# Optimization experiments

Measured on AMD Instinct MI355X. Metric: run time of the kernel, lower is better.

The kernel has to match this reference:

```python
import jax, jax.numpy as jnp
import numpy as np

C = 1.0          # curvature
MIN_NORM = 1e-15
EPS = 1e-7       # atanh clamp for fp32

def _sqnorm(x):
    return jnp.sum(x * x, axis=-1, keepdims=True)

def _norm(x):
    return jnp.sqrt(jnp.maximum(_sqnorm(x), MIN_NORM))

def _atanh(u):
    return jnp.arctanh(jnp.clip(u, -1.0 + EPS, 1.0 - EPS))

def mobius_add(x, y, c):
    x2 = _sqnorm(x); y2 = _sqnorm(y)
    xy = jnp.sum(x * y, axis=-1, keepdims=True)
    num = (1.0 + 2.0 * c * xy + c * y2) * x + (1.0 - c * x2) * y
    den = 1.0 + 2.0 * c * xy + c * c * x2 * y2
    return num / jnp.maximum(den, MIN_NORM)

def logmap0(p, c):
    sc = jnp.sqrt(c)
    pn = _norm(p)
    return p / pn / sc * _atanh(sc * pn)

def logmap(p1, p2, c):
    # tangent vector at p1 pointing to p2 (Poincare ball)
    sub = mobius_add(-p1, p2, c)
    sn = _norm(sub)
    lam = 2.0 / jnp.maximum(1.0 - c * _sqnorm(p1), MIN_NORM)
    sc = jnp.sqrt(c)
    return 2.0 / sc / lam * _atanh(sc * sn) * sub / sn

def expmap(p, u, c):
    un = _norm(u)
    lam = 2.0 / jnp.maximum(1.0 - c * _sqnorm(p), MIN_NORM)
    sc = jnp.sqrt(c)
    second = jnp.tanh(sc * lam * un / 2.0) * u / (sc * un)
    return mobius_add(p, second, c)


def setup_inputs() -> dict:
    key = jax.random.key(0)
    k1, k2, k3 = jax.random.split(key, 3)
    B, N, D = 1, 1024, 128
    # points inside the unit Poincare ball (||x|| ~ 0.23)
    x = jax.random.normal(k1, (B, N, D), jnp.float32) * 0.02
    # sparse-ish dense adjacency mask (0/1 floats)
    adj = (jax.random.uniform(k2, (B, N, N)) < 0.05).astype(jnp.float32)
    # DenseAtt: nn.Linear(2*D, 1) weight (flattened) + bias
    att_w = jax.random.normal(k3, (2 * D,), jnp.float32) * 0.1
    att_b = jnp.zeros((), jnp.float32)
    return {"x": x, "adj": adj, "att_w": att_w, "att_b": att_b}


def reference(x, adj, att_w, att_b):
    B, N, D = x.shape
    x_t = logmap0(x, C)                                   # [B,N,D]
    # DenseAtt: sigmoid(Linear(cat(x_i, x_j))) decomposed as left_i + right_j + b
    left = x_t @ att_w[:D]                                # [B,N]
    right = x_t @ att_w[D:]                               # [B,N]
    att = jax.nn.sigmoid(left[:, :, None] + right[:, None, :] + att_b) * adj  # [B,N,N]
    # pairwise logmap: tangent at x_i of every x_j  -> [B,N,N,D]
    x_local = logmap(x[:, :, None, :], x[:, None, :, :], C)
    support_t = jnp.einsum('bij,bijd->bid', att, x_local)  # [B,N,D]
    return expmap(x, support_t, C)
```

## Files before the change

### kernel.cpp

```cpp
#include <hip/hip_runtime.h>
#include <math.h>


typedef short short4v __attribute__((ext_vector_type(4)));
typedef short short8v __attribute__((ext_vector_type(8)));
typedef float float4v __attribute__((ext_vector_type(4)));

static __device__ __forceinline__ short f2bf(float f) {
    unsigned u = __float_as_uint(f);
    u += 0x7fff + ((u >> 16) & 1);
    return (short)(u >> 16);
}
static __device__ __forceinline__ float rcpf(float x) { return __builtin_amdgcn_rcpf(x); }
static __device__ __forceinline__ short8v ld8(const unsigned short* p) {
    short4v lo = *(const short4v*)p;
    short4v hi = *(const short4v*)(p + 4);
    return (short8v){lo[0],lo[1],lo[2],lo[3],hi[0],hi[1],hi[2],hi[3]};
}
static __device__ __forceinline__ float dot4(float4v a, float4v b) {
    return a[0]*b[0] + a[1]*b[1] + a[2]*b[2] + a[3]*b[3];
}
static __device__ __forceinline__ float atanh_over(float pn) {
    float uu = fminf(pn, 1.f - 1e-7f);
    return 0.5f * __logf((1.f + uu) * rcpf(1.f - uu)) * rcpf(pn);
}

__global__ __launch_bounds__(256) void hyp_prep(
    const float* __restrict__ x, const float* __restrict__ w,
    const float* __restrict__ battp,
    unsigned short* __restrict__ Xb, unsigned short* __restrict__ Xbt,
    float* __restrict__ st_x2, float* __restrict__ st_L, float* __restrict__ st_R)
{
    __shared__ unsigned short sT[128 * 20];
    __shared__ float sPx[16 * 36], sPl[16 * 36], sPr[16 * 36];
    const int t  = threadIdx.x;
    const int r0 = blockIdx.x * 16;
    const float4v* x4 = (const float4v*)x;
    const float4v* w4 = (const float4v*)w;

#pragma unroll
    for (int it = 0; it < 2; ++it) {
        int bid = t + it * 256;
        int jr = bid >> 5, dc = bid & 31;
        float4v v  = x4[(r0 + jr) * 32 + dc];
        float4v w1 = w4[dc], w2 = w4[32 + dc];
        short4v h = { f2bf(v[0]), f2bf(v[1]), f2bf(v[2]), f2bf(v[3]) };
        *(short4v*)&Xb[(r0 + jr) * 128 + dc * 4] = h;
#pragma unroll
        for (int d = 0; d < 4; ++d)
            sT[(dc * 4 + d) * 20 + jr] = (unsigned short)h[d];
        sPx[jr * 36 + dc] = dot4(v, v);
        sPl[jr * 36 + dc] = dot4(v, w1);
        sPr[jr * 36 + dc] = dot4(v, w2);
    }
    __syncthreads();
    {
        int dim = t >> 1, h = t & 1;
        short8v vv = ld8(&sT[dim * 20 + h * 8]);
        *(short8v*)&Xbt[dim * 1024 + r0 + h * 8] = vv;
    }
    if (t < 16) {
        float x2 = 0.f, l = 0.f, r = 0.f;
#pragma unroll
        for (int k = 0; k < 8; ++k) {
            float4v a = *(float4v*)&sPx[t * 36 + k * 4];
            float4v b = *(float4v*)&sPl[t * 36 + k * 4];
            float4v c = *(float4v*)&sPr[t * 36 + k * 4];
            x2 += a[0] + a[1] + a[2] + a[3];
            l  += b[0] + b[1] + b[2] + b[3];
            r  += c[0] + c[1] + c[2] + c[3];
        }
        float pn = sqrtf(fmaxf(x2, 1e-15f));
        float f  = atanh_over(pn);
        st_x2[r0 + t] = x2;
        st_L [r0 + t] = l * f + battp[0];
        st_R [r0 + t] = r * f;
    }
}

__global__ __launch_bounds__(256, 4) void hyp_pair(
    const unsigned short* __restrict__ Xb, const unsigned short* __restrict__ Xbt,
    const float* __restrict__ adj,
    const float* __restrict__ st_x2, const float* __restrict__ st_L,
    const float* __restrict__ st_R,
    float* __restrict__ Yp, float* __restrict__ Sp)
{
    __shared__ unsigned short sW[16 * 68];
    __shared__ float sSp[4 * 256];

    const int t    = threadIdx.x;
    const int lane = t & 63;
    const int wave = t >> 6;
    const int n    = lane & 15;
    const int q    = lane >> 4;
    const int i0   = blockIdx.x * 16;
    const int c    = blockIdx.y;
    const int j0   = c * 64;
    const int jrow = j0 + wave * 16 + n;

    float x2j = st_x2[jrow];
    float rj  = st_R[jrow];
    float x2i4[4], li4[4], bi4[4], adjv[4];
#pragma unroll
    for (int r = 0; r < 4; ++r) {
        int i = i0 + q * 4 + r;
        x2i4[r] = st_x2[i];
        li4[r]  = st_L[i];
        adjv[r] = adj[i * 1024 + jrow];
    }
    short8v afrag[4], bfA[4];
#pragma unroll
    for (int kk = 0; kk < 4; ++kk) {
        afrag[kk] = *(const short8v*)&Xb[(i0 + n) * 128 + kk * 32 + q * 8];
        bfA  [kk] = *(const short8v*)&Xb[jrow * 128     + kk * 32 + q * 8];
    }
    short8v bfB[2][2];
#pragma unroll
    for (int nsl = 0; nsl < 2; ++nsl) {
        int ns = wave * 2 + nsl;
#pragma unroll
        for (int kk = 0; kk < 2; ++kk)
            bfB[nsl][kk] = *(const short8v*)&Xbt[(ns * 16 + n) * 1024 + j0 + kk * 32 + q * 8];
    }
#pragma unroll
    for (int r = 0; r < 4; ++r) bi4[r] = 1.f - x2i4[r];

    float4v acc = (float4v){0.f, 0.f, 0.f, 0.f};
#pragma unroll
    for (int kk = 0; kk < 4; ++kk)
        acc = __builtin_amdgcn_mfma_f32_16x16x32_bf16(afrag[kk], bfA[kk], acc, 0, 0, 0);

    float Sacc[4];
#pragma unroll
    for (int r = 0; r < 4; ++r) {
        float G     = acc[r];
        float alpha = 1.f - 2.f * G + x2j;
        float den   = fmaxf(fmaf(x2i4[r], x2j, 1.f - 2.f * G), 1e-15f);
        float rdn   = rcpf(den);
        float bb    = bi4[r];
        float nn2   = alpha * alpha * x2i4[r] + bb * bb * x2j - 2.f * alpha * bb * G;
        float sn    = sqrtf(fmaxf(nn2 * rdn * rdn, 1e-15f));
        float tt    = atanh_over(sn);
        float z     = li4[r] + rj;
        float sig   = rcpf(1.f + __expf(-z));
        float g     = sig * adjv[r] * tt * rdn;
        Sacc[r]     = g * alpha;
        sW[(q * 4 + r) * 68 + wave * 16 + n] = (unsigned short)f2bf(g);
    }
    __syncthreads();

    float4v accB[2];
    accB[0] = (float4v){0.f, 0.f, 0.f, 0.f};
    accB[1] = (float4v){0.f, 0.f, 0.f, 0.f};
#pragma unroll
    for (int nsl = 0; nsl < 2; ++nsl) {
#pragma unroll
        for (int kk = 0; kk < 2; ++kk) {
            short8v a = ld8(&sW[n * 68 + kk * 32 + q * 8]);
            accB[nsl] = __builtin_amdgcn_mfma_f32_16x16x32_bf16(a, bfB[nsl][kk], accB[nsl], 0, 0, 0);
        }
    }

    float* Yc = Yp + c * 131072;
#pragma unroll
    for (int nsl = 0; nsl < 2; ++nsl) {
        int ns = wave * 2 + nsl;
#pragma unroll
        for (int r = 0; r < 4; ++r)
            Yc[(i0 + q * 4 + r) * 128 + ns * 16 + n] = accB[nsl][r];
    }
#pragma unroll
    for (int r = 0; r < 4; ++r)
        sSp[wave * 256 + (q * 4 + r) * 16 + n] = Sacc[r];
    __syncthreads();
    if (t < 16) {
        float s = 0.f;
#pragma unroll
        for (int wv = 0; wv < 4; ++wv)
#pragma unroll
            for (int k4 = 0; k4 < 4; ++k4) {
                float4v v = *(float4v*)&sSp[wv * 256 + t * 16 + k4 * 4];
                s += v[0] + v[1] + v[2] + v[3];
            }
        Sp[c * 1024 + i0 + t] = s;
    }
}

__global__ __launch_bounds__(256) void hyp_exp(
    const float* __restrict__ x, const float* __restrict__ Yp,
    const float* __restrict__ Sp, const float* __restrict__ st_x2,
    float* __restrict__ out)
{
    const int t   = threadIdx.x;
    const int row = blockIdx.x * 8 + (t >> 5);
    const int l32 = t & 31;
    float4v y = (float4v){0.f, 0.f, 0.f, 0.f};
    float S = 0.f;
#pragma unroll
    for (int c = 0; c < 16; ++c) {
        y += *(const float4v*)&Yp[c * 131072 + row * 128 + l32 * 4];
        S += Sp[c * 1024 + row];
    }
    float4v xa = ((const float4v*)x)[row * 32 + l32];
    float x2 = st_x2[row];
    float bE = fmaxf(1.f - x2, 1e-15f);
    float u[4], un2p = 0.f, xup = 0.f;
#pragma unroll
    for (int e = 0; e < 4; ++e) {
        u[e] = bE * (bE * y[e] - S * xa[e]);
        un2p += u[e] * u[e];
        xup  += xa[e] * u[e];
    }
#pragma unroll
    for (int m = 1; m < 32; m <<= 1) {
        un2p += __shfl_xor(un2p, m, 32);
        xup  += __shfl_xor(xup,  m, 32);
    }
    float un  = sqrtf(fmaxf(un2p, 1e-15f));
    float e2  = __expf(2.f * un * rcpf(bE));
    float th  = 1.f - 2.f * rcpf(e2 + 1.f);
    float s2  = th * rcpf(un);
    float xy  = s2 * xup;
    float y2s = th * th;
    float coef = 1.f + 2.f * xy + y2s;
    float den  = fmaxf(1.f + 2.f * xy + x2 * y2s, 1e-15f);
    float rd   = rcpf(den);
    float4v o = { (coef*xa[0] + bE*s2*u[0])*rd, (coef*xa[1] + bE*s2*u[1])*rd,
                  (coef*xa[2] + bE*s2*u[2])*rd, (coef*xa[3] + bE*s2*u[3])*rd };
    ((float4v*)out)[row * 32 + l32] = o;
}

extern "C" void kernel_launch(void* const* d_in, const int* in_sizes, int n_in,
                              void* d_out, int out_size, void* d_ws, size_t ws_size,
                              hipStream_t stream) {
    const float* x    = (const float*)d_in[0];
    const float* adj  = (const float*)d_in[1];
    const float* w    = (const float*)d_in[2];
    const float* batt = (const float*)d_in[3];
    float* out = (float*)d_out;

    float* Yp    = (float*)d_ws;
    float* Sp    = Yp + 16 * 131072;
    float* st_x2 = Sp + 16 * 1024;
    float* st_L  = st_x2 + 1024;
    float* st_R  = st_L + 1024;
    unsigned short* Xb  = (unsigned short*)(st_R + 1024);
    unsigned short* Xbt = Xb + 1024 * 128;

    hipLaunchKernelGGL(hyp_prep, dim3(64), dim3(256), 0, stream,
                       x, w, batt, Xb, Xbt, st_x2, st_L, st_R);
    hipLaunchKernelGGL(hyp_pair, dim3(64, 16), dim3(256), 0, stream,
                       Xb, Xbt, adj, st_x2, st_L, st_R, Yp, Sp);
    hipLaunchKernelGGL(hyp_exp, dim3(128), dim3(256), 0, stream,
                       x, Yp, Sp, st_x2, out);
}
```

Measured before the change: 77.03 us.

## Fuse prep kernel into pairwise kernel, recomputing per-row stats per block

```diff
diff --git a/kernel.cpp b/kernel.cpp
--- a/kernel.cpp
+++ b/kernel.cpp
@@ -10,6 +10,9 @@
     unsigned u = __float_as_uint(f);
     u += 0x7fff + ((u >> 16) & 1);
     return (short)(u >> 16);
+}
+static __device__ __forceinline__ float bf2f(unsigned short s) {
+    return __uint_as_float(((unsigned)s) << 16);
 }
 static __device__ __forceinline__ float rcpf(float x) { return __builtin_amdgcn_rcpf(x); }
 static __device__ __forceinline__ short8v ld8(const unsigned short* p) {
@@ -25,67 +28,19 @@
     return 0.5f * __logf((1.f + uu) * rcpf(1.f - uu)) * rcpf(pn);
 }
 
-__global__ __launch_bounds__(256) void hyp_prep(
-    const float* __restrict__ x, const float* __restrict__ w,
-    const float* __restrict__ battp,
-    unsigned short* __restrict__ Xb, unsigned short* __restrict__ Xbt,
-    float* __restrict__ st_x2, float* __restrict__ st_L, float* __restrict__ st_R)
-{
-    __shared__ unsigned short sT[128 * 20];
-    __shared__ float sPx[16 * 36], sPl[16 * 36], sPr[16 * 36];
-    const int t  = threadIdx.x;
-    const int r0 = blockIdx.x * 16;
-    const float4v* x4 = (const float4v*)x;
-    const float4v* w4 = (const float4v*)w;
-
-#pragma unroll
-    for (int it = 0; it < 2; ++it) {
-        int bid = t + it * 256;
-        int jr = bid >> 5, dc = bid & 31;
-        float4v v  = x4[(r0 + jr) * 32 + dc];
-        float4v w1 = w4[dc], w2 = w4[32 + dc];
-        short4v h = { f2bf(v[0]), f2bf(v[1]), f2bf(v[2]), f2bf(v[3]) };
-        *(short4v*)&Xb[(r0 + jr) * 128 + dc * 4] = h;
-#pragma unroll
-        for (int d = 0; d < 4; ++d)
-            sT[(dc * 4 + d) * 20 + jr] = (unsigned short)h[d];
-        sPx[jr * 36 + dc] = dot4(v, v);
-        sPl[jr * 36 + dc] = dot4(v, w1);
-        sPr[jr * 36 + dc] = dot4(v, w2);
-    }
-    __syncthreads();
-    {
-        int dim = t >> 1, h = t & 1;
-        short8v vv = ld8(&sT[dim * 20 + h * 8]);
-        *(short8v*)&Xbt[dim * 1024 + r0 + h * 8] = vv;
-    }
-    if (t < 16) {
-        float x2 = 0.f, l = 0.f, r = 0.f;
-#pragma unroll
-        for (int k = 0; k < 8; ++k) {
-            float4v a = *(float4v*)&sPx[t * 36 + k * 4];
-            float4v b = *(float4v*)&sPl[t * 36 + k * 4];
-            float4v c = *(float4v*)&sPr[t * 36 + k * 4];
-            x2 += a[0] + a[1] + a[2] + a[3];
-            l  += b[0] + b[1] + b[2] + b[3];
-            r  += c[0] + c[1] + c[2] + c[3];
-        }
-        float pn = sqrtf(fmaxf(x2, 1e-15f));
-        float f  = atanh_over(pn);
-        st_x2[r0 + t] = x2;
-        st_L [r0 + t] = l * f + battp[0];
-        st_R [r0 + t] = r * f;
-    }
-}
-
-__global__ __launch_bounds__(256, 4) void hyp_pair(
-    const unsigned short* __restrict__ Xb, const unsigned short* __restrict__ Xbt,
-    const float* __restrict__ adj,
-    const float* __restrict__ st_x2, const float* __restrict__ st_L,
-    const float* __restrict__ st_R,
+__global__ __launch_bounds__(256, 4) void hyp_main(
+    const float* __restrict__ x, const float* __restrict__ adj,
+    const float* __restrict__ battp, const float* __restrict__ w,
     float* __restrict__ Yp, float* __restrict__ Sp)
 {
-    __shared__ unsigned short sW[16 * 68];
+    __shared__ unsigned short sXI[16 * 132];
+    __shared__ unsigned short sXJ[64 * 132];
+    __shared__ unsigned short sW [16 * 68];
+    __shared__ float sW2f[128];
+    __shared__ float sPx[128], sPr[128];
+    __shared__ float sPxI[64], sPlI[64];
+    __shared__ float sX2J[64], sRJ[64];
+    __shared__ float sX2I[16], sLI[16];
     __shared__ float sSp[4 * 256];
 
     const int t    = threadIdx.x;
@@ -97,38 +52,122 @@
     const int c    = blockIdx.y;
     const int j0   = c * 64;
     const int jrow = j0 + wave * 16 + n;
-
-    float x2j = st_x2[jrow];
-    float rj  = st_R[jrow];
-    float x2i4[4], li4[4], bi4[4], adjv[4];
+    const float batt = battp[0];
+
+    const float4v* x4 = (const float4v*)x;
+    const float4v* w4 = (const float4v*)w;
+
+    float adjv[4];
+#pragma unroll
+    for (int r = 0; r < 4; ++r)
+        adjv[r] = adj[(i0 + q * 4 + r) * 1024 + jrow];
+
+    float fB[2][2][8];
+#pragma unroll
+    for (int nsl = 0; nsl < 2; ++nsl) {
+        int d0 = (wave * 2 + nsl) * 16 + n;
+#pragma unroll
+        for (int kk = 0; kk < 2; ++kk)
+#pragma unroll
+            for (int e = 0; e < 8; ++e)
+                fB[nsl][kk][e] = x[(j0 + kk * 32 + q * 8 + e) * 128 + d0];
+    }
+
+    if (t < 32) *(float4v*)&sW2f[t * 4] = w4[32 + t];
+    if (t < 64) {
+        int i = t >> 2, qt = t & 3;
+        float x2p = 0.f, lp = 0.f;
+#pragma unroll
+        for (int k = 0; k < 8; ++k) {
+            float4v v  = x4[(i0 + i) * 32 + qt * 8 + k];
+            float4v wv = w4[qt * 8 + k];
+            x2p += dot4(v, v);
+            lp  += dot4(v, wv);
+        }
+        sPxI[t] = x2p; sPlI[t] = lp;
+    }
+#pragma unroll
+    for (int it = 0; it < 2; ++it) {
+        int idx = t + it * 256;
+        int r = idx >> 5, cc = idx & 31;
+        float4v v = x4[(i0 + r) * 32 + cc];
+        short4v h = { f2bf(v[0]), f2bf(v[1]), f2bf(v[2]), f2bf(v[3]) };
+        *(short4v*)&sXI[r * 132 + cc * 4] = h;
+    }
+#pragma unroll
+    for (int it = 0; it < 8; ++it) {
+        int idx = t + it * 256;
+        int r = idx >> 5, cc = idx & 31;
+        float4v v = x4[(j0 + r) * 32 + cc];
+        short4v h = { f2bf(v[0]), f2bf(v[1]), f2bf(v[2]), f2bf(v[3]) };
+        *(short4v*)&sXJ[r * 132 + cc * 4] = h;
+    }
+    __syncthreads();
+
+    if (t < 128) {
+        int j = t >> 1, half = t & 1;
+        const unsigned short* rowp = &sXJ[j * 132 + half * 64];
+        float x2p = 0.f, rp = 0.f;
+#pragma unroll
+        for (int k = 0; k < 8; ++k) {
+            short8v v = ld8(rowp + k * 8);
+#pragma unroll
+            for (int e = 0; e < 8; ++e) {
+                float f = bf2f((unsigned short)v[e]);
+                x2p = fmaf(f, f, x2p);
+                rp  = fmaf(f, sW2f[half * 64 + k * 8 + e], rp);
+            }
+        }
+        sPx[t] = x2p; sPr[t] = rp;
+    }
+    short8v bfB[2][2];
+#pragma unroll
+    for (int nsl = 0; nsl < 2; ++nsl)
+#pragma unroll
+        for (int kk = 0; kk < 2; ++kk) {
+            short8v h;
+#pragma unroll
+            for (int e = 0; e < 8; ++e) h[e] = f2bf(fB[nsl][kk][e]);
+            bfB[nsl][kk] = h;
+        }
+    __syncthreads();
+
+    if (t < 64) {
+        float x2 = sPx[2 * t] + sPx[2 * t + 1];
+        float r  = sPr[2 * t] + sPr[2 * t + 1];
+        float pn = sqrtf(fmaxf(x2, 1e-15f));
+        sX2J[t] = x2;
+        sRJ[t]  = r * atanh_over(pn);
+    } else if (t < 80) {
+        int i = t - 64;
+        float x2 = sPxI[4*i] + sPxI[4*i+1] + sPxI[4*i+2] + sPxI[4*i+3];
+        float l  = sPlI[4*i] + sPlI[4*i+1] + sPlI[4*i+2] + sPlI[4*i+3];
+        float pn = sqrtf(fmaxf(x2, 1e-15f));
+        sX2I[i] = x2;
+        sLI[i]  = l * atanh_over(pn) + batt;
+    }
+    __syncthreads();
+
+    float x2i4[4], bi4[4], li4[4];
 #pragma unroll
     for (int r = 0; r < 4; ++r) {
-        int i = i0 + q * 4 + r;
-        x2i4[r] = st_x2[i];
-        li4[r]  = st_L[i];
-        adjv[r] = adj[i * 1024 + jrow];
-    }
-    short8v afrag[4], bfA[4];
+        x2i4[r] = sX2I[q * 4 + r];
+        li4[r]  = sLI[q * 4 + r];
+        bi4[r]  = 1.f - x2i4[r];
+    }
+    float x2j = sX2J[wave * 16 + n];
+    float rj  = sRJ [wave * 16 + n];
+    short8v afrag[4];
+#pragma unroll
+    for (int kk = 0; kk < 4; ++kk)
+        afrag[kk] = ld8(&sXI[n * 132 + kk * 32 + q * 8]);
+
+    float4v acc = (float4v){0.f, 0.f, 0.f, 0.f};
 #pragma unroll
     for (int kk = 0; kk < 4; ++kk) {
-        afrag[kk] = *(const short8v*)&Xb[(i0 + n) * 128 + kk * 32 + q * 8];
-        bfA  [kk] = *(const short8v*)&Xb[jrow * 128     + kk * 32 + q * 8];
-    }
-    short8v bfB[2][2];
-#pragma unroll
-    for (int nsl = 0; nsl < 2; ++nsl) {
-        int ns = wave * 2 + nsl;
-#pragma unroll
-        for (int kk = 0; kk < 2; ++kk)
-            bfB[nsl][kk] = *(const short8v*)&Xbt[(ns * 16 + n) * 1024 + j0 + kk * 32 + q * 8];
-    }
-#pragma unroll
-    for (int r = 0; r < 4; ++r) bi4[r] = 1.f - x2i4[r];
-
-    float4v acc = (float4v){0.f, 0.f, 0.f, 0.f};
-#pragma unroll
-    for (int kk = 0; kk < 4; ++kk)
-        acc = __builtin_amdgcn_mfma_f32_16x16x32_bf16(afrag[kk], bfA[kk], acc, 0, 0, 0);
+        short8v b = ld8(&sXJ[(wave * 16 + n) * 132 + kk * 32 + q * 8]);
+        acc = __builtin_amdgcn_mfma_f32_16x16x32_bf16(afrag[kk], b, acc, 0, 0, 0);
+    }
 
     float Sacc[4];
 #pragma unroll
@@ -153,21 +192,20 @@
     accB[0] = (float4v){0.f, 0.f, 0.f, 0.f};
     accB[1] = (float4v){0.f, 0.f, 0.f, 0.f};
 #pragma unroll
-    for (int nsl = 0; nsl < 2; ++nsl) {
+    for (int nsl = 0; nsl < 2; ++nsl)
 #pragma unroll
         for (int kk = 0; kk < 2; ++kk) {
             short8v a = ld8(&sW[n * 68 + kk * 32 + q * 8]);
             accB[nsl] = __builtin_amdgcn_mfma_f32_16x16x32_bf16(a, bfB[nsl][kk], accB[nsl], 0, 0, 0);
         }
-    }
 
     float* Yc = Yp + c * 131072;
 #pragma unroll
     for (int nsl = 0; nsl < 2; ++nsl) {
-        int ns = wave * 2 + nsl;
+        int d0 = (wave * 2 + nsl) * 16 + n;
 #pragma unroll
         for (int r = 0; r < 4; ++r)
-            Yc[(i0 + q * 4 + r) * 128 + ns * 16 + n] = accB[nsl][r];
+            Yc[(i0 + q * 4 + r) * 128 + d0] = accB[nsl][r];
     }
 #pragma unroll
     for (int r = 0; r < 4; ++r)
@@ -188,8 +226,7 @@
 
 __global__ __launch_bounds__(256) void hyp_exp(
     const float* __restrict__ x, const float* __restrict__ Yp,
-    const float* __restrict__ Sp, const float* __restrict__ st_x2,
-    float* __restrict__ out)
+    const float* __restrict__ Sp, float* __restrict__ out)
 {
     const int t   = threadIdx.x;
     const int row = blockIdx.x * 8 + (t >> 5);
@@ -202,8 +239,10 @@
         S += Sp[c * 1024 + row];
     }
     float4v xa = ((const float4v*)x)[row * 32 + l32];
-    float x2 = st_x2[row];
-    float bE = fmaxf(1.f - x2, 1e-15f);
+    float x2p = dot4(xa, xa);
+#pragma unroll
+    for (int m = 1; m < 32; m <<= 1) x2p += __shfl_xor(x2p, m, 32);
+    float bE = fmaxf(1.f - x2p, 1e-15f);
     float u[4], un2p = 0.f, xup = 0.f;
 #pragma unroll
     for (int e = 0; e < 4; ++e) {
@@ -223,7 +262,7 @@
     float xy  = s2 * xup;
     float y2s = th * th;
     float coef = 1.f + 2.f * xy + y2s;
-    float den  = fmaxf(1.f + 2.f * xy + x2 * y2s, 1e-15f);
+    float den  = fmaxf(1.f + 2.f * xy + x2p * y2s, 1e-15f);
     float rd   = rcpf(den);
     float4v o = { (coef*xa[0] + bE*s2*u[0])*rd, (coef*xa[1] + bE*s2*u[1])*rd,
                   (coef*xa[2] + bE*s2*u[2])*rd, (coef*xa[3] + bE*s2*u[3])*rd };
@@ -239,18 +278,10 @@
     const float* batt = (const float*)d_in[3];
     float* out = (float*)d_out;
 
-    float* Yp    = (float*)d_ws;
-    float* Sp    = Yp + 16 * 131072;
-    float* st_x2 = Sp + 16 * 1024;
-    float* st_L  = st_x2 + 1024;
-    float* st_R  = st_L + 1024;
-    unsigned short* Xb  = (unsigned short*)(st_R + 1024);
-    unsigned short* Xbt = Xb + 1024 * 128;
-
-    hipLaunchKernelGGL(hyp_prep, dim3(64), dim3(256), 0, stream,
-                       x, w, batt, Xb, Xbt, st_x2, st_L, st_R);
-    hipLaunchKernelGGL(hyp_pair, dim3(64, 16), dim3(256), 0, stream,
-                       Xb, Xbt, adj, st_x2, st_L, st_R, Yp, Sp);
-    hipLaunchKernelGGL(hyp_exp, dim3(128), dim3(256), 0, stream,
-                       x, Yp, Sp, st_x2, out);
-}
+    float* Yp = (float*)d_ws;
+    float* Sp = Yp + 16 * 131072;
+
+    hipLaunchKernelGGL(hyp_main, dim3(64, 16), dim3(256), 0, stream,
+                       x, adj, batt, w, Yp, Sp);
+    hipLaunchKernelGGL(hyp_exp, dim3(128), dim3(256), 0, stream, x, Yp, Sp, out);
+}
```

After: 76.51 us. About the same (-0.7%).
